# Kernel tuning notes

Hardware: AMD Instinct MI355X
Metric: run time of the kernel (lower is better)

The kernel has to match this reference:

```python
import jax, jax.numpy as jnp
import numpy as np

EMBED_DIM = 1024
NUM_HEADS = 16
HEAD_DIM = EMBED_DIM // NUM_HEADS
BATCH = 2
SEQ = 2048


def setup_inputs() -> dict:
    key = jax.random.key(0)
    ks = jax.random.split(key, 9)
    s = 1.0 / np.sqrt(EMBED_DIM)
    x = jax.random.normal(ks[0], (BATCH, SEQ, EMBED_DIM), dtype=jnp.float32)
    Wq = jax.random.uniform(ks[1], (EMBED_DIM, EMBED_DIM), jnp.float32, -s, s)
    bq = jax.random.uniform(ks[2], (EMBED_DIM,), jnp.float32, -s, s)
    Wk = jax.random.uniform(ks[3], (EMBED_DIM, EMBED_DIM), jnp.float32, -s, s)
    bk = jax.random.uniform(ks[4], (EMBED_DIM,), jnp.float32, -s, s)
    Wv = jax.random.uniform(ks[5], (EMBED_DIM, EMBED_DIM), jnp.float32, -s, s)
    bv = jax.random.uniform(ks[6], (EMBED_DIM,), jnp.float32, -s, s)
    Wo = jax.random.uniform(ks[7], (EMBED_DIM, EMBED_DIM), jnp.float32, -s, s)
    bo = jax.random.uniform(ks[8], (EMBED_DIM,), jnp.float32, -s, s)
    return {"x": x, "Wq": Wq, "bq": bq, "Wk": Wk, "bk": bk,
            "Wv": Wv, "bv": bv, "Wo": Wo, "bo": bo}


def reference(x, Wq, bq, Wk, bk, Wv, bv, Wo, bo):
    B, S, E = x.shape
    H, D = NUM_HEADS, HEAD_DIM

    def split_heads(t):
        # [B, S, E] -> [B, H, S, D]
        return t.reshape(B, S, H, D).transpose(0, 2, 1, 3)

    q = split_heads(x @ Wq + bq)
    k = split_heads(x @ Wk + bk)
    v = split_heads(x @ Wv + bv)

    scale = 1.0 / np.sqrt(D).astype(np.float32)
    scores = jnp.einsum('bhqd,bhkd->bhqk', q, k) * scale  # [B,H,S,S]
    attn = jax.nn.softmax(scores, axis=-1)
    out = jnp.einsum('bhqk,bhkd->bhqd', attn, v)  # [B,H,S,D]
    out = out.transpose(0, 2, 1, 3).reshape(B, S, E)
    return out @ Wo + bo
```

## Files before the change

### kernel.cpp

```cpp
#include <hip/hip_runtime.h>
#include <cstdint>

#define BATCH 2
#define SEQ   2048
#define EMB   1024
#define NHEAD 16
#define HDIM  64
#define NTOK  (BATCH*SEQ)

typedef __attribute__((ext_vector_type(8))) short bf16x8;
typedef __attribute__((ext_vector_type(8))) short short8;
typedef __attribute__((ext_vector_type(4))) float f32x4;

__device__ inline unsigned short f2bf(float f) {
    unsigned u = __float_as_uint(f);
    u += 0x7FFF + ((u >> 16) & 1);
    return (unsigned short)(u >> 16);
}

__device__ inline unsigned cvt_pk_bf16(float lo, float hi) {
    unsigned r;
    asm("v_cvt_pk_bf16_f32 %0, %1, %2" : "=v"(r) : "v"(lo), "v"(hi));
    return r;
}

__device__ inline void gload16(const void* g, void* lds) {
    __builtin_amdgcn_global_load_lds(
        (const __attribute__((address_space(1))) unsigned int*)g,
        (__attribute__((address_space(3))) unsigned int*)lds, 16, 0, 0);
}

__global__ __launch_bounds__(256)
void conv_x(const float* __restrict__ x, unsigned short* __restrict__ xb) {
    int i = (blockIdx.x * 256 + threadIdx.x) * 8;
    float4 a = *(const float4*)(x + i);
    float4 b = *(const float4*)(x + i + 4);
    short8 o;
    o[0]=f2bf(a.x); o[1]=f2bf(a.y); o[2]=f2bf(a.z); o[3]=f2bf(a.w);
    o[4]=f2bf(b.x); o[5]=f2bf(b.y); o[6]=f2bf(b.z); o[7]=f2bf(b.w);
    *(short8*)(xb + i) = o;
}

__global__ __launch_bounds__(256)
void conv_wt(const float* __restrict__ Wq, const float* __restrict__ Wk,
             const float* __restrict__ Wv, const float* __restrict__ Wo,
             unsigned short* __restrict__ Wt) {
    const float* W = blockIdx.z==0?Wq : blockIdx.z==1?Wk : blockIdx.z==2?Wv : Wo;
    unsigned short* out = Wt + (size_t)blockIdx.z * EMB * EMB;
    __shared__ float T[64][68];
    const int t = threadIdx.x;
    const int k0 = blockIdx.x * 64, n0 = blockIdx.y * 64;
    #pragma unroll
    for (int rr = 0; rr < 4; ++rr) {
        int row = (t >> 4) + 16 * rr;
        float4 v = *(const float4*)(W + (size_t)(k0+row)*EMB + n0 + (t&15)*4);
        *(float4*)&T[row][(t&15)*4] = v;
    }
    __syncthreads();
    #pragma unroll
    for (int it = 0; it < 2; ++it) {
        int ci = it*256 + t;
        int nr = ci >> 3, kc = ci & 7;
        short8 o;
        #pragma unroll
        for (int j = 0; j < 8; ++j) o[j] = f2bf(T[kc*8+j][nr]);
        *(short8*)(out + (size_t)(n0+nr)*EMB + k0 + kc*8) = o;
    }
}

__global__ __launch_bounds__(256)
void transpose_v(const unsigned short* __restrict__ Vb, unsigned short* __restrict__ Vt) {
    __shared__ unsigned short T[64*65];
    const int t = threadIdx.x;
    const int s0 = blockIdx.x * 64;
    const int bh = blockIdx.y;
    const int b = bh >> 4, h = bh & 15;
    const unsigned short* src = Vb + ((size_t)b*SEQ + s0)*EMB + h*HDIM;
    #pragma unroll
    for (int it = 0; it < 2; ++it) {
        int ci = it*256 + t;
        int r = ci >> 3, c = ci & 7;
        short8 v = *(const short8*)(src + (size_t)r*EMB + c*8);
        #pragma unroll
        for (int j = 0; j < 8; ++j) T[r*65 + c*8 + j] = (unsigned short)v[j];
    }
    __syncthreads();
    unsigned short* dst = Vt + (size_t)bh * HDIM * SEQ + s0;
    #pragma unroll
    for (int it = 0; it < 2; ++it) {
        int ci = it*256 + t;
        int d = ci >> 3, c = ci & 7;
        short8 o;
        #pragma unroll
        for (int j = 0; j < 8; ++j) o[j] = (short)T[(c*8 + j)*65 + d];
        *(short8*)(dst + (size_t)d*SEQ + c*8) = o;
    }
}

__global__ __launch_bounds__(256)
void gemm_qkv(const unsigned short* __restrict__ xb, const unsigned short* __restrict__ Wt,
              const float* __restrict__ bq, const float* __restrict__ bk,
              const float* __restrict__ bv,
              unsigned short* __restrict__ Qb, unsigned short* __restrict__ Kb,
              unsigned short* __restrict__ Vb) {
    const int z = blockIdx.z;
    const unsigned short* W = Wt + (size_t)z * EMB * EMB;
    const float* bias = z==0 ? bq : z==1 ? bk : bv;
    unsigned short* out = z==0 ? Qb : z==1 ? Kb : Vb;
    const float scale = z==0 ? (0.125f * 1.44269504f) : 1.0f;

    __shared__ __align__(16) unsigned short As[2][128*32];
    __shared__ __align__(16) unsigned short Bs[2][128*32];

    const int tid = threadIdx.x, lane = tid & 63, wid = tid >> 6;
    const int m0 = blockIdx.y * 128, n0 = blockIdx.x * 128;
    const int wr = wid >> 1, wc = wid & 1;

    const int ci0 = tid, ci1 = 256 + tid;
    const int row0 = ci0 >> 2, c0 = (ci0 & 3) ^ ((row0 >> 1) & 3);
    const int row1 = ci1 >> 2, c1 = (ci1 & 3) ^ ((row1 >> 1) & 3);
    const int dst0 = wid*64, dst1 = 256 + wid*64;

    f32x4 acc[4][4];
    #pragma unroll
    for (int i = 0; i < 4; ++i)
        #pragma unroll
        for (int j = 0; j < 4; ++j) acc[i][j] = f32x4{0.f,0.f,0.f,0.f};

    gload16(xb + (size_t)(m0+row0)*EMB + c0*8, (char*)As[0] + dst0*16);
    gload16(W  + (size_t)(n0+row0)*EMB + c0*8, (char*)Bs[0] + dst0*16);
    gload16(xb + (size_t)(m0+row1)*EMB + c1*8, (char*)As[0] + dst1*16);
    gload16(W  + (size_t)(n0+row1)*EMB + c1*8, (char*)Bs[0] + dst1*16);
    __syncthreads();

    for (int kk = 0; kk < EMB/32; ++kk) {
        const int cur = kk & 1;
        if (kk < EMB/32 - 1) {
            int k0 = (kk+1) * 32;
            gload16(xb + (size_t)(m0+row0)*EMB + k0 + c0*8, (char*)As[cur^1] + dst0*16);
            gload16(W  + (size_t)(n0+row0)*EMB + k0 + c0*8, (char*)Bs[cur^1] + dst0*16);
            gload16(xb + (size_t)(m0+row1)*EMB + k0 + c1*8, (char*)As[cur^1] + dst1*16);
            gload16(W  + (size_t)(n0+row1)*EMB + k0 + c1*8, (char*)Bs[cur^1] + dst1*16);
        }
        bf16x8 af[4], bf[4];
        #pragma unroll
        for (int i = 0; i < 4; ++i) {
            int ar = 64*wr + 16*i + (lane & 15);
            int ac = (lane >> 4) ^ ((ar >> 1) & 3);
            af[i] = *(const bf16x8*)((const char*)As[cur] + ar*64 + ac*16);
            int br = 64*wc + 16*i + (lane & 15);
            int bc = (lane >> 4) ^ ((br >> 1) & 3);
            bf[i] = *(const bf16x8*)((const char*)Bs[cur] + br*64 + bc*16);
        }
        __builtin_amdgcn_s_setprio(1);
        #pragma unroll
        for (int i = 0; i < 4; ++i)
            #pragma unroll
            for (int j = 0; j < 4; ++j)
                acc[i][j] = __builtin_amdgcn_mfma_f32_16x16x32_bf16(af[i], bf[j], acc[i][j], 0, 0, 0);
        __builtin_amdgcn_s_setprio(0);
        __syncthreads();
    }

    #pragma unroll
    for (int j = 0; j < 4; ++j) {
        int col = n0 + 64*wc + 16*j + (lane & 15);
        float bvv = bias[col];
        #pragma unroll
        for (int i = 0; i < 4; ++i) {
            int rw0 = m0 + 64*wr + 16*i + (lane >> 4) * 4;
            #pragma unroll
            for (int r = 0; r < 4; ++r)
                out[(size_t)(rw0+r)*EMB + col] = f2bf((acc[i][j][r] + bvv) * scale);
        }
    }
}

__global__ __launch_bounds__(256)
void gemm_out(const unsigned short* __restrict__ Cb, const unsigned short* __restrict__ Wto,
              const float* __restrict__ bo, float* __restrict__ out) {
    __shared__ __align__(16) unsigned short As[2][64*32];
    __shared__ __align__(16) unsigned short Bs[2][128*32];

    const int tid = threadIdx.x, lane = tid & 63, wid = tid >> 6;
    const int m0 = blockIdx.y * 64, n0 = blockIdx.x * 128;
    const int wr = wid >> 1, wc = wid & 1;

    const int arow_ = tid >> 2, ac_ = (tid & 3) ^ ((arow_ >> 1) & 3);
    const int ci1 = 256 + tid;
    const int brow0 = tid >> 2, bc0 = (tid & 3) ^ ((brow0 >> 1) & 3);
    const int brow1 = ci1 >> 2, bc1 = (ci1 & 3) ^ ((brow1 >> 1) & 3);
    const int dst0 = wid*64, dst1 = 256 + wid*64;

    f32x4 acc[2][4];
    #pragma unroll
    for (int i = 0; i < 2; ++i)
        #pragma unroll
        for (int j = 0; j < 4; ++j) acc[i][j] = f32x4{0.f,0.f,0.f,0.f};

    gload16(Cb  + (size_t)(m0+arow_)*EMB + ac_*8, (char*)As[0] + dst0*16);
    gload16(Wto + (size_t)(n0+brow0)*EMB + bc0*8, (char*)Bs[0] + dst0*16);
    gload16(Wto + (size_t)(n0+brow1)*EMB + bc1*8, (char*)Bs[0] + dst1*16);
    __syncthreads();

    for (int kk = 0; kk < EMB/32; ++kk) {
        const int cur = kk & 1;
        if (kk < EMB/32 - 1) {
            int k0 = (kk+1) * 32;
            gload16(Cb  + (size_t)(m0+arow_)*EMB + k0 + ac_*8, (char*)As[cur^1] + dst0*16);
            gload16(Wto + (size_t)(n0+brow0)*EMB + k0 + bc0*8, (char*)Bs[cur^1] + dst0*16);
            gload16(Wto + (size_t)(n0+brow1)*EMB + k0 + bc1*8, (char*)Bs[cur^1] + dst1*16);
        }
        bf16x8 af[2], bf[4];
        #pragma unroll
        for (int i = 0; i < 2; ++i) {
            int ar = 32*wr + 16*i + (lane & 15);
            int ac = (lane >> 4) ^ ((ar >> 1) & 3);
            af[i] = *(const bf16x8*)((const char*)As[cur] + ar*64 + ac*16);
        }
        #pragma unroll
        for (int j = 0; j < 4; ++j) {
            int br = 64*wc + 16*j + (lane & 15);
            int bc = (lane >> 4) ^ ((br >> 1) & 3);
            bf[j] = *(const bf16x8*)((const char*)Bs[cur] + br*64 + bc*16);
        }
        __builtin_amdgcn_s_setprio(1);
        #pragma unroll
        for (int i = 0; i < 2; ++i)
            #pragma unroll
            for (int j = 0; j < 4; ++j)
                acc[i][j] = __builtin_amdgcn_mfma_f32_16x16x32_bf16(af[i], bf[j], acc[i][j], 0, 0, 0);
        __builtin_amdgcn_s_setprio(0);
        __syncthreads();
    }

    #pragma unroll
    for (int j = 0; j < 4; ++j) {
        int col = n0 + 64*wc + 16*j + (lane & 15);
        float bvv = bo[col];
        #pragma unroll
        for (int i = 0; i < 2; ++i) {
            int row0 = m0 + 32*wr + 16*i + (lane >> 4) * 4;
            #pragma unroll
            for (int r = 0; r < 4; ++r)
                out[(size_t)(row0+r)*EMB + col] = acc[i][j][r] + bvv;
        }
    }
}

__global__ __launch_bounds__(256, 4)
void attn(const unsigned short* __restrict__ Qg, const unsigned short* __restrict__ Kg,
          const unsigned short* __restrict__ Vt, unsigned short* __restrict__ Cg) {
    __shared__ __align__(16) unsigned short Ks[2][64*64];
    __shared__ __align__(16) unsigned short Vs[2][64*64];

    const int tid = threadIdx.x, lane = tid & 63, wid = tid >> 6;
    const int qb = blockIdx.x, bh = blockIdx.y;
    const int b = bh >> 4, h = bh & 15;
    const size_t base = (size_t)b * SEQ * EMB + (size_t)h * HDIM;
    const unsigned short* Qp = Qg + base + (size_t)qb * 64 * EMB;
    const unsigned short* Kp = Kg + base;
    const unsigned short* Vtp = Vt + (size_t)bh * HDIM * SEQ;

    #pragma unroll
    for (int it = 0; it < 2; ++it) {
        int ci = it*256 + tid, row = ci >> 3, c = (ci & 7) ^ (row & 7);
        gload16(Qp + (size_t)row*EMB + c*8, (char*)Ks[0] + (it*256 + wid*64)*16);
    }
    __syncthreads();
    bf16x8 qf[2];
    #pragma unroll
    for (int kc = 0; kc < 2; ++kc) {
        int r = 16*wid + (lane & 15);
        int c = ((lane >> 4) + 4*kc) ^ (r & 7);
        qf[kc] = *(const bf16x8*)((const char*)Ks[0] + r*128 + c*16);
    }
    __syncthreads();

    #pragma unroll
    for (int it = 0; it < 2; ++it) {
        int ci = it*256 + tid, row = ci >> 3, c = (ci & 7) ^ (row & 7);
        gload16(Kp + (size_t)row*EMB + c*8, (char*)Ks[0] + (it*256 + wid*64)*16);
        gload16(Vtp + (size_t)row*SEQ + c*8, (char*)Vs[0] + (it*256 + wid*64)*16);
    }
    __syncthreads();

    f32x4 O[4];
    #pragma unroll
    for (int j = 0; j < 4; ++j) O[j] = f32x4{0.f,0.f,0.f,0.f};
    float l_run = 0.f;

    for (int kt = 0; kt < SEQ/64; ++kt) {
        const int cur = kt & 1, nxt = cur ^ 1;
        if (kt < SEQ/64 - 1) {
            const unsigned short* Kt = Kp + (size_t)(kt+1)*64*EMB;
            const unsigned short* Vn = Vtp + (size_t)(kt+1)*64;
            #pragma unroll
            for (int it = 0; it < 2; ++it) {
                int ci = it*256 + tid, row = ci >> 3, c = (ci & 7) ^ (row & 7);
                gload16(Kt + (size_t)row*EMB + c*8, (char*)Ks[nxt] + (it*256 + wid*64)*16);
                gload16(Vn + (size_t)row*SEQ + c*8, (char*)Vs[nxt] + (it*256 + wid*64)*16);
            }
        }

        f32x4 s[4];
        __builtin_amdgcn_s_setprio(1);
        #pragma unroll
        for (int nk = 0; nk < 4; ++nk) {
            s[nk] = f32x4{0.f,0.f,0.f,0.f};
            #pragma unroll
            for (int kc = 0; kc < 2; ++kc) {
                int r = 16*nk + (lane & 15);
                int c = ((lane >> 4) + 4*kc) ^ (r & 7);
                bf16x8 kf = *(const bf16x8*)((const char*)Ks[cur] + r*128 + c*16);
                s[nk] = __builtin_amdgcn_mfma_f32_16x16x32_bf16(kf, qf[kc], s[nk], 0, 0, 0);
            }
        }
        __builtin_amdgcn_s_setprio(0);

        float psv[4];
        #pragma unroll
        for (int nk = 0; nk < 4; ++nk) {
            #pragma unroll
            for (int r = 0; r < 4; ++r)
                s[nk][r] = exp2f(s[nk][r]);
            psv[nk] = (s[nk][0] + s[nk][1]) + (s[nk][2] + s[nk][3]);
        }
        float ps = (psv[0] + psv[1]) + (psv[2] + psv[3]);
        ps += __shfl_xor(ps, 16);
        ps += __shfl_xor(ps, 32);
        l_run += ps;

        unsigned pk[4][2];
        #pragma unroll
        for (int nk = 0; nk < 4; ++nk) {
            pk[nk][0] = cvt_pk_bf16(s[nk][0], s[nk][1]);
            pk[nk][1] = cvt_pk_bf16(s[nk][2], s[nk][3]);
        }
        const int hh = lane >> 4;
        const int srcA = (((hh << 1) & 3) << 4) | (lane & 15);
        const int srcB = srcA + 16;
        const int hs = hh >> 1;
        bf16x8 pf[2];
        #pragma unroll
        for (int kc = 0; kc < 2; ++kc) {
            union { unsigned u[4]; bf16x8 v; } cvt;
            unsigned a0 = __shfl((int)pk[2*kc][0], srcA), b0 = __shfl((int)pk[2*kc+1][0], srcA);
            cvt.u[0] = hs ? b0 : a0;
            unsigned a1 = __shfl((int)pk[2*kc][1], srcA), b1 = __shfl((int)pk[2*kc+1][1], srcA);
            cvt.u[1] = hs ? b1 : a1;
            unsigned a2 = __shfl((int)pk[2*kc][0], srcB), b2 = __shfl((int)pk[2*kc+1][0], srcB);
            cvt.u[2] = hs ? b2 : a2;
            unsigned a3 = __shfl((int)pk[2*kc][1], srcB), b3 = __shfl((int)pk[2*kc+1][1], srcB);
            cvt.u[3] = hs ? b3 : a3;
            pf[kc] = cvt.v;
        }

        __builtin_amdgcn_s_setprio(1);
        #pragma unroll
        for (int jd = 0; jd < 4; ++jd) {
            #pragma unroll
            for (int kc = 0; kc < 2; ++kc) {
                int d = 16*jd + (lane & 15);
                int c = ((lane >> 4) + 4*kc) ^ (d & 7);
                bf16x8 vf = *(const bf16x8*)((const char*)Vs[cur] + d*128 + c*16);
                O[jd] = __builtin_amdgcn_mfma_f32_16x16x32_bf16(pf[kc], vf, O[jd], 0, 0, 0);
            }
        }
        __builtin_amdgcn_s_setprio(0);
        __syncthreads();
    }

    float inv[4];
    #pragma unroll
    for (int r = 0; r < 4; ++r) inv[r] = 1.f / __shfl(l_run, (lane >> 4)*4 + r);
    unsigned short* Cp = Cg + base + (size_t)qb * 64 * EMB;
    #pragma unroll
    for (int jd = 0; jd < 4; ++jd)
        #pragma unroll
        for (int r = 0; r < 4; ++r) {
            int row = 16*wid + (lane >> 4)*4 + r;
            int col = 16*jd + (lane & 15);
            Cp[(size_t)row*EMB + col] = f2bf(O[jd][r] * inv[r]);
        }
}

extern "C" void kernel_launch(void* const* d_in, const int* in_sizes, int n_in,
                              void* d_out, int out_size, void* d_ws, size_t ws_size,
                              hipStream_t stream) {
    const float* x  = (const float*)d_in[0];
    const float* Wq = (const float*)d_in[1];
    const float* bq = (const float*)d_in[2];
    const float* Wk = (const float*)d_in[3];
    const float* bk = (const float*)d_in[4];
    const float* Wv = (const float*)d_in[5];
    const float* bv = (const float*)d_in[6];
    const float* Wo = (const float*)d_in[7];
    const float* bo = (const float*)d_in[8];
    float* out = (float*)d_out;

    unsigned short* xb = (unsigned short*)d_ws;
    unsigned short* Wt = xb + (size_t)NTOK * EMB;
    unsigned short* Qb = Wt + (size_t)4 * EMB * EMB;
    unsigned short* Kb = Qb + (size_t)NTOK * EMB;
    unsigned short* Vb = Kb + (size_t)NTOK * EMB;
    unsigned short* Cb = Vb + (size_t)NTOK * EMB;
    unsigned short* Vtr = Cb + (size_t)NTOK * EMB;

    conv_x<<<dim3((NTOK*EMB)/(256*8)), 256, 0, stream>>>(x, xb);
    conv_wt<<<dim3(16, 16, 4), 256, 0, stream>>>(Wq, Wk, Wv, Wo, Wt);
    gemm_qkv<<<dim3(8, 32, 3), 256, 0, stream>>>(xb, Wt, bq, bk, bv, Qb, Kb, Vb);
    transpose_v<<<dim3(SEQ/64, BATCH*NHEAD), 256, 0, stream>>>(Vb, Vtr);
    attn<<<dim3(SEQ/64, BATCH*NHEAD), 256, 0, stream>>>(Qb, Kb, Vtr, Cb);
    gemm_out<<<dim3(EMB/128, NTOK/64), 256, 0, stream>>>(Cb, Wt + (size_t)3*EMB*EMB, bo, out);
}
```

Measured before the change: 219.9 us.

## Split-K output GEMM with atomics, flatten QKV grid, use permlane swaps in attention

The output projection now uses 128x128 tiles with a two-way split over K. Partial sums are combined with float atomicAdd into an output that is first zeroed by a memset. The QKV GEMM grid is flattened so the projection index comes from blockIdx.x, and setprio hints are dropped from both GEMMs. In attention, the shuffle-based P re-layout is replaced with v_permlane32/16_swap instructions to cut cross-lane shuffle cost. The split-K path adds a memset and atomic traffic, and makes the summation order nondeterministic.

```diff
diff --git a/kernel.cpp b/kernel.cpp
--- a/kernel.cpp
+++ b/kernel.cpp
@@ -103,17 +103,19 @@
               const float* __restrict__ bv,
               unsigned short* __restrict__ Qb, unsigned short* __restrict__ Kb,
               unsigned short* __restrict__ Vb) {
-    const int z = blockIdx.z;
+    const int bx = blockIdx.x;
+    const int z = bx >> 3;
     const unsigned short* W = Wt + (size_t)z * EMB * EMB;
     const float* bias = z==0 ? bq : z==1 ? bk : bv;
     unsigned short* out = z==0 ? Qb : z==1 ? Kb : Vb;
     const float scale = z==0 ? (0.125f * 1.44269504f) : 1.0f;
+    const int nL = (bx & 7) * 128;
 
     __shared__ __align__(16) unsigned short As[2][128*32];
     __shared__ __align__(16) unsigned short Bs[2][128*32];
 
     const int tid = threadIdx.x, lane = tid & 63, wid = tid >> 6;
-    const int m0 = blockIdx.y * 128, n0 = blockIdx.x * 128;
+    const int m0 = blockIdx.y * 128;
     const int wr = wid >> 1, wc = wid & 1;
 
     const int ci0 = tid, ci1 = 256 + tid;
@@ -128,9 +130,9 @@
         for (int j = 0; j < 4; ++j) acc[i][j] = f32x4{0.f,0.f,0.f,0.f};
 
     gload16(xb + (size_t)(m0+row0)*EMB + c0*8, (char*)As[0] + dst0*16);
-    gload16(W  + (size_t)(n0+row0)*EMB + c0*8, (char*)Bs[0] + dst0*16);
+    gload16(W  + (size_t)(nL+row0)*EMB + c0*8, (char*)Bs[0] + dst0*16);
     gload16(xb + (size_t)(m0+row1)*EMB + c1*8, (char*)As[0] + dst1*16);
-    gload16(W  + (size_t)(n0+row1)*EMB + c1*8, (char*)Bs[0] + dst1*16);
+    gload16(W  + (size_t)(nL+row1)*EMB + c1*8, (char*)Bs[0] + dst1*16);
     __syncthreads();
 
     for (int kk = 0; kk < EMB/32; ++kk) {
@@ -138,9 +140,9 @@
         if (kk < EMB/32 - 1) {
             int k0 = (kk+1) * 32;
             gload16(xb + (size_t)(m0+row0)*EMB + k0 + c0*8, (char*)As[cur^1] + dst0*16);
-            gload16(W  + (size_t)(n0+row0)*EMB + k0 + c0*8, (char*)Bs[cur^1] + dst0*16);
+            gload16(W  + (size_t)(nL+row0)*EMB + k0 + c0*8, (char*)Bs[cur^1] + dst0*16);
             gload16(xb + (size_t)(m0+row1)*EMB + k0 + c1*8, (char*)As[cur^1] + dst1*16);
-            gload16(W  + (size_t)(n0+row1)*EMB + k0 + c1*8, (char*)Bs[cur^1] + dst1*16);
+            gload16(W  + (size_t)(nL+row1)*EMB + k0 + c1*8, (char*)Bs[cur^1] + dst1*16);
         }
         bf16x8 af[4], bf[4];
         #pragma unroll
@@ -152,19 +154,17 @@
             int bc = (lane >> 4) ^ ((br >> 1) & 3);
             bf[i] = *(const bf16x8*)((const char*)Bs[cur] + br*64 + bc*16);
         }
-        __builtin_amdgcn_s_setprio(1);
         #pragma unroll
         for (int i = 0; i < 4; ++i)
             #pragma unroll
             for (int j = 0; j < 4; ++j)
                 acc[i][j] = __builtin_amdgcn_mfma_f32_16x16x32_bf16(af[i], bf[j], acc[i][j], 0, 0, 0);
-        __builtin_amdgcn_s_setprio(0);
         __syncthreads();
     }
 
     #pragma unroll
     for (int j = 0; j < 4; ++j) {
-        int col = n0 + 64*wc + 16*j + (lane & 15);
+        int col = nL + 64*wc + 16*j + (lane & 15);
         float bvv = bias[col];
         #pragma unroll
         for (int i = 0; i < 4; ++i) {
@@ -179,71 +179,69 @@
 __global__ __launch_bounds__(256)
 void gemm_out(const unsigned short* __restrict__ Cb, const unsigned short* __restrict__ Wto,
               const float* __restrict__ bo, float* __restrict__ out) {
-    __shared__ __align__(16) unsigned short As[2][64*32];
+    __shared__ __align__(16) unsigned short As[2][128*32];
     __shared__ __align__(16) unsigned short Bs[2][128*32];
 
     const int tid = threadIdx.x, lane = tid & 63, wid = tid >> 6;
-    const int m0 = blockIdx.y * 64, n0 = blockIdx.x * 128;
+    const int m0 = blockIdx.y * 128, n0 = blockIdx.x * 128;
+    const int kb = blockIdx.z * (EMB/2);
     const int wr = wid >> 1, wc = wid & 1;
 
-    const int arow_ = tid >> 2, ac_ = (tid & 3) ^ ((arow_ >> 1) & 3);
-    const int ci1 = 256 + tid;
-    const int brow0 = tid >> 2, bc0 = (tid & 3) ^ ((brow0 >> 1) & 3);
-    const int brow1 = ci1 >> 2, bc1 = (ci1 & 3) ^ ((brow1 >> 1) & 3);
+    const int ci0 = tid, ci1 = 256 + tid;
+    const int row0 = ci0 >> 2, c0 = (ci0 & 3) ^ ((row0 >> 1) & 3);
+    const int row1 = ci1 >> 2, c1 = (ci1 & 3) ^ ((row1 >> 1) & 3);
     const int dst0 = wid*64, dst1 = 256 + wid*64;
 
-    f32x4 acc[2][4];
-    #pragma unroll
-    for (int i = 0; i < 2; ++i)
+    f32x4 acc[4][4];
+    #pragma unroll
+    for (int i = 0; i < 4; ++i)
         #pragma unroll
         for (int j = 0; j < 4; ++j) acc[i][j] = f32x4{0.f,0.f,0.f,0.f};
 
-    gload16(Cb  + (size_t)(m0+arow_)*EMB + ac_*8, (char*)As[0] + dst0*16);
-    gload16(Wto + (size_t)(n0+brow0)*EMB + bc0*8, (char*)Bs[0] + dst0*16);
-    gload16(Wto + (size_t)(n0+brow1)*EMB + bc1*8, (char*)Bs[0] + dst1*16);
-    __syncthreads();
-
-    for (int kk = 0; kk < EMB/32; ++kk) {
+    gload16(Cb  + (size_t)(m0+row0)*EMB + kb + c0*8, (char*)As[0] + dst0*16);
+    gload16(Wto + (size_t)(n0+row0)*EMB + kb + c0*8, (char*)Bs[0] + dst0*16);
+    gload16(Cb  + (size_t)(m0+row1)*EMB + kb + c1*8, (char*)As[0] + dst1*16);
+    gload16(Wto + (size_t)(n0+row1)*EMB + kb + c1*8, (char*)Bs[0] + dst1*16);
+    __syncthreads();
+
+    for (int kk = 0; kk < EMB/64; ++kk) {
         const int cur = kk & 1;
-        if (kk < EMB/32 - 1) {
-            int k0 = (kk+1) * 32;
-            gload16(Cb  + (size_t)(m0+arow_)*EMB + k0 + ac_*8, (char*)As[cur^1] + dst0*16);
-            gload16(Wto + (size_t)(n0+brow0)*EMB + k0 + bc0*8, (char*)Bs[cur^1] + dst0*16);
-            gload16(Wto + (size_t)(n0+brow1)*EMB + k0 + bc1*8, (char*)Bs[cur^1] + dst1*16);
-        }
-        bf16x8 af[2], bf[4];
-        #pragma unroll
-        for (int i = 0; i < 2; ++i) {
-            int ar = 32*wr + 16*i + (lane & 15);
+        if (kk < EMB/64 - 1) {
+            int k0 = kb + (kk+1) * 32;
+            gload16(Cb  + (size_t)(m0+row0)*EMB + k0 + c0*8, (char*)As[cur^1] + dst0*16);
+            gload16(Wto + (size_t)(n0+row0)*EMB + k0 + c0*8, (char*)Bs[cur^1] + dst0*16);
+            gload16(Cb  + (size_t)(m0+row1)*EMB + k0 + c1*8, (char*)As[cur^1] + dst1*16);
+            gload16(Wto + (size_t)(n0+row1)*EMB + k0 + c1*8, (char*)Bs[cur^1] + dst1*16);
+        }
+        bf16x8 af[4], bf[4];
+        #pragma unroll
+        for (int i = 0; i < 4; ++i) {
+            int ar = 64*wr + 16*i + (lane & 15);
             int ac = (lane >> 4) ^ ((ar >> 1) & 3);
             af[i] = *(const bf16x8*)((const char*)As[cur] + ar*64 + ac*16);
-        }
-        #pragma unroll
-        for (int j = 0; j < 4; ++j) {
-            int br = 64*wc + 16*j + (lane & 15);
+            int br = 64*wc + 16*i + (lane & 15);
             int bc = (lane >> 4) ^ ((br >> 1) & 3);
-            bf[j] = *(const bf16x8*)((const char*)Bs[cur] + br*64 + bc*16);
-        }
-        __builtin_amdgcn_s_setprio(1);
-        #pragma unroll
-        for (int i = 0; i < 2; ++i)
+            bf[i] = *(const bf16x8*)((const char*)Bs[cur] + br*64 + bc*16);
+        }
+        #pragma unroll
+        for (int i = 0; i < 4; ++i)
             #pragma unroll
             for (int j = 0; j < 4; ++j)
                 acc[i][j] = __builtin_amdgcn_mfma_f32_16x16x32_bf16(af[i], bf[j], acc[i][j], 0, 0, 0);
-        __builtin_amdgcn_s_setprio(0);
         __syncthreads();
     }
 
+    const bool first = (blockIdx.z == 0);
     #pragma unroll
     for (int j = 0; j < 4; ++j) {
         int col = n0 + 64*wc + 16*j + (lane & 15);
-        float bvv = bo[col];
-        #pragma unroll
-        for (int i = 0; i < 2; ++i) {
-            int row0 = m0 + 32*wr + 16*i + (lane >> 4) * 4;
+        float bvv = first ? bo[col] : 0.0f;
+        #pragma unroll
+        for (int i = 0; i < 4; ++i) {
+            int rw0 = m0 + 64*wr + 16*i + (lane >> 4) * 4;
             #pragma unroll
             for (int r = 0; r < 4; ++r)
-                out[(size_t)(row0+r)*EMB + col] = acc[i][j][r] + bvv;
+                atomicAdd(&out[(size_t)(rw0+r)*EMB + col], acc[i][j][r] + bvv);
         }
     }
 }
@@ -337,22 +335,17 @@
             pk[nk][0] = cvt_pk_bf16(s[nk][0], s[nk][1]);
             pk[nk][1] = cvt_pk_bf16(s[nk][2], s[nk][3]);
         }
-        const int hh = lane >> 4;
-        const int srcA = (((hh << 1) & 3) << 4) | (lane & 15);
-        const int srcB = srcA + 16;
-        const int hs = hh >> 1;
         bf16x8 pf[2];
         #pragma unroll
         for (int kc = 0; kc < 2; ++kc) {
+            unsigned x0 = pk[2*kc][0],   y0 = pk[2*kc+1][0];
+            unsigned x1 = pk[2*kc][1],   y1 = pk[2*kc+1][1];
+            asm("v_permlane32_swap_b32 %0, %1" : "+v"(x0), "+v"(y0));
+            asm("v_permlane16_swap_b32 %0, %1" : "+v"(x0), "+v"(y0));
+            asm("v_permlane32_swap_b32 %0, %1" : "+v"(x1), "+v"(y1));
+            asm("v_permlane16_swap_b32 %0, %1" : "+v"(x1), "+v"(y1));
             union { unsigned u[4]; bf16x8 v; } cvt;
-            unsigned a0 = __shfl((int)pk[2*kc][0], srcA), b0 = __shfl((int)pk[2*kc+1][0], srcA);
-            cvt.u[0] = hs ? b0 : a0;
-            unsigned a1 = __shfl((int)pk[2*kc][1], srcA), b1 = __shfl((int)pk[2*kc+1][1], srcA);
-            cvt.u[1] = hs ? b1 : a1;
-            unsigned a2 = __shfl((int)pk[2*kc][0], srcB), b2 = __shfl((int)pk[2*kc+1][0], srcB);
-            cvt.u[2] = hs ? b2 : a2;
-            unsigned a3 = __shfl((int)pk[2*kc][1], srcB), b3 = __shfl((int)pk[2*kc+1][1], srcB);
-            cvt.u[3] = hs ? b3 : a3;
+            cvt.u[0] = x0; cvt.u[1] = x1; cvt.u[2] = y0; cvt.u[3] = y1;
             pf[kc] = cvt.v;
         }
 
@@ -407,10 +400,11 @@
     unsigned short* Cb = Vb + (size_t)NTOK * EMB;
     unsigned short* Vtr = Cb + (size_t)NTOK * EMB;
 
+    hipMemsetAsync(out, 0, (size_t)out_size * sizeof(float), stream);
     conv_x<<<dim3((NTOK*EMB)/(256*8)), 256, 0, stream>>>(x, xb);
     conv_wt<<<dim3(16, 16, 4), 256, 0, stream>>>(Wq, Wk, Wv, Wo, Wt);
-    gemm_qkv<<<dim3(8, 32, 3), 256, 0, stream>>>(xb, Wt, bq, bk, bv, Qb, Kb, Vb);
+    gemm_qkv<<<dim3(24, 32), 256, 0, stream>>>(xb, Wt, bq, bk, bv, Qb, Kb, Vb);
     transpose_v<<<dim3(SEQ/64, BATCH*NHEAD), 256, 0, stream>>>(Vb, Vtr);
     attn<<<dim3(SEQ/64, BATCH*NHEAD), 256, 0, stream>>>(Qb, Kb, Vtr, Cb);
-    gemm_out<<<dim3(EMB/128, NTOK/64), 256, 0, stream>>>(Cb, Wt + (size_t)3*EMB*EMB, bo, out);
-}
+    gemm_out<<<dim3(EMB/128, NTOK/128, 2), 256, 0, stream>>>(Cb, Wt + (size_t)3*EMB*EMB, bo, out);
+}
```

Measured after the change: 239.1 us. +8.7%, slower.
